# Performance work log

Measured on AMD Instinct MI355X. Metric: run time of the kernel, lower is better.

The kernel has to match this reference:

```python
import jax, jax.numpy as jnp
import numpy as np

B, L, C, H = 2, 4096, 1024, 16
D = C // H
KERNEL_FROM_KN = lambda kn: int(np.sqrt(kn)) + 1


def setup_inputs() -> dict:
    key = jax.random.key(0)
    ks = jax.random.split(key, 4)
    s = 0.02
    kk = KERNEL_FROM_KN(144)  # 13
    return {
        "x": jax.random.normal(ks[0], (B, L, C), jnp.float32),
        "w_qkv": jax.random.normal(ks[1], (C, 3 * C), jnp.float32) * s,
        "b_qkv": jnp.zeros((3 * C,), jnp.float32),
        "rpb": jax.random.normal(ks[2], (H, 2 * kk - 1), jnp.float32) * s,
        "w_proj": jax.random.normal(ks[3], (C, C), jnp.float32) * s,
        "b_proj": jnp.zeros((C,), jnp.float32),
        "k_neighbors": 144,
    }


def reference(x, w_qkv, b_qkv, rpb, w_proj, b_proj, k_neighbors):
    kk = KERNEL_FROM_KN(k_neighbors)  # kernel size (13)
    scale = D ** -0.5
    qkv = (x @ w_qkv + b_qkv).reshape(B, L, 3, H, D).transpose(2, 0, 3, 1, 4)  # (3,B,H,L,D)
    q, k, v = qkv[0] * scale, qkv[1], qkv[2]
    pos = jnp.arange(L)
    # NATTEN window: centered, clamped so the full kernel fits inside [0, L)
    start = jnp.clip(pos - kk // 2, 0, L - kk)               # (L,)
    idx = start[:, None] + jnp.arange(kk)[None, :]           # (L,kk) key positions
    k_win = k[:, :, idx, :]                                  # (B,H,L,kk,D)
    v_win = v[:, :, idx, :]                                  # (B,H,L,kk,D)
    attn = jnp.einsum('bhld,bhlkd->bhlk', q, k_win)          # (B,H,L,kk)
    # relative-position bias index = key_pos - query_pos + (kk - 1) in [0, 2kk-2]
    bias_idx = idx - pos[:, None] + (kk - 1)                 # (L,kk)
    attn = attn + rpb[:, bias_idx][None]                     # broadcast over batch
    attn = jax.nn.softmax(attn, axis=-1)
    out = jnp.einsum('bhlk,bhlkd->bhld', attn, v_win)        # (B,H,L,D)
    out = out.transpose(0, 2, 1, 3).reshape(B, L, C)
    return out @ w_proj + b_proj
```

## Files before the change

kernel.cpp:

```cpp
#include <hip/hip_runtime.h>
#include <hip/hip_bf16.h>
#include <stdint.h>

typedef __bf16 bf16x8 __attribute__((ext_vector_type(8)));
typedef float floatx4 __attribute__((ext_vector_type(4)));

#define B_ 2
#define L_ 4096
#define C_ 1024
#define H_ 16
#define D_ 64
constexpr size_t TEN = (size_t)B_ * H_ * L_ * D_;

__device__ __forceinline__ float bf2f(unsigned short u) {
  union { unsigned int i; float f; } x; x.i = ((unsigned int)u) << 16; return x.f;
}
__device__ __forceinline__ unsigned short f2bf(float f) {
  union { float f; unsigned int i; } x; x.f = f;
  unsigned int i = x.i;
  return (unsigned short)((i + 0x7FFFu + ((i >> 16) & 1u)) >> 16);
}

__device__ __forceinline__ void async_copy16(const unsigned short* g, unsigned short* l) {
  __builtin_amdgcn_global_load_lds(
      (const __attribute__((address_space(1))) unsigned int*)g,
      (__attribute__((address_space(3))) unsigned int*)l,
      16, 0, 0);
}

__global__ __launch_bounds__(256) void cvt_f32_bf16_kernel(
    const float* __restrict__ in, unsigned short* __restrict__ out, int n) {
  int i = (blockIdx.x * 256 + threadIdx.x) * 8;
  if (i >= n) return;
  float4 a = *(const float4*)&in[i];
  float4 b = *(const float4*)&in[i + 4];
  union { uint4 u; unsigned short s[8]; } st;
  st.s[0] = f2bf(a.x); st.s[1] = f2bf(a.y); st.s[2] = f2bf(a.z); st.s[3] = f2bf(a.w);
  st.s[4] = f2bf(b.x); st.s[5] = f2bf(b.y); st.s[6] = f2bf(b.z); st.s[7] = f2bf(b.w);
  *(uint4*)&out[i] = st.u;
}

__global__ __launch_bounds__(256) void transpose_f32_bf16(
    const float* __restrict__ in, unsigned short* __restrict__ out,
    int R, int Ccols) {
  __shared__ float tile[64][65];
  const int bx = blockIdx.x * 64;
  const int by = blockIdx.y * 64;
  const int t = threadIdx.x;
  for (int i = t; i < 1024; i += 256) {
    int r = i >> 4, c4 = (i & 15) << 2;
    float4 v = *(const float4*)&in[(size_t)(by + r) * Ccols + bx + c4];
    tile[r][c4] = v.x; tile[r][c4 + 1] = v.y; tile[r][c4 + 2] = v.z; tile[r][c4 + 3] = v.w;
  }
  __syncthreads();
  for (int i = t; i < 512; i += 256) {
    int r = i >> 3, c8 = (i & 7) << 3;
    union { uint4 u; unsigned short s[8]; } st;
    #pragma unroll
    for (int j = 0; j < 8; ++j) st.s[j] = f2bf(tile[c8 + j][r]);
    *(uint4*)&out[(size_t)(bx + r) * R + by + c8] = st.u;
  }
}

template <int MODE>
__global__ __launch_bounds__(256) void gemm_bt_kernel(
    const unsigned short* __restrict__ A, const unsigned short* __restrict__ Bt,
    const float* __restrict__ bias, unsigned short* __restrict__ out_bf,
    float* __restrict__ out_f, int M, int N, int K, float qscale) {
  constexpr int BK = 64;
  __shared__ unsigned short a_sh[128 * BK];
  __shared__ unsigned short b_sh[128 * BK];

  const int t = threadIdx.x;
  const int nwgx = gridDim.x;
  const int nwg = nwgx * gridDim.y;
  const int flat = blockIdx.y * nwgx + blockIdx.x;
  const int cpx = nwg >> 3;
  const int swz = (flat & 7) * cpx + (flat >> 3);
  const int n0 = (swz % nwgx) * 128;
  const int m0 = (swz / nwgx) * 128;

  const int wave = t >> 6, lane = t & 63;
  const int wr = wave >> 1, wc = wave & 1;
  const int lm = lane & 15, quad = lane >> 4;

  const int soff = t * 8;
  const int srow = soff >> 6;
  const int scol = soff & 63;

  floatx4 acc[4][4];
  #pragma unroll
  for (int i = 0; i < 4; ++i)
    #pragma unroll
    for (int j = 0; j < 4; ++j) acc[i][j] = (floatx4)0.0f;

  for (int kt = 0; kt < K; kt += BK) {
    #pragma unroll
    for (int p = 0; p < 4; ++p) {
      int r = srow + p * 32;
      int c = scol ^ ((r & 7) << 3);
      int off = r * BK + scol;
      async_copy16(&A[(size_t)(m0 + r) * K + kt + c], &a_sh[off]);
      async_copy16(&Bt[(size_t)(n0 + r) * K + kt + c], &b_sh[off]);
    }
    __syncthreads();
    #pragma unroll
    for (int ks = 0; ks < BK; ks += 32) {
      bf16x8 af[4], bfr[4];
      #pragma unroll
      for (int i = 0; i < 4; ++i) {
        int ra = wr * 64 + i * 16 + lm;
        af[i] = *(const bf16x8*)&a_sh[ra * BK + ((ks + quad * 8) ^ ((ra & 7) << 3))];
      }
      #pragma unroll
      for (int j = 0; j < 4; ++j) {
        int rb = wc * 64 + j * 16 + lm;
        bfr[j] = *(const bf16x8*)&b_sh[rb * BK + ((ks + quad * 8) ^ ((rb & 7) << 3))];
      }
      #pragma unroll
      for (int i = 0; i < 4; ++i)
        #pragma unroll
        for (int j = 0; j < 4; ++j)
          acc[i][j] = __builtin_amdgcn_mfma_f32_16x16x32_bf16(af[i], bfr[j], acc[i][j], 0, 0, 0);
    }
    __syncthreads();
  }

  #pragma unroll
  for (int j = 0; j < 4; ++j) {
    int col = n0 + wc * 64 + j * 16 + lm;
    float bv = bias[col];
    if (MODE == 0) {
      int which = col >> 10;
      int rem = col & 1023;
      int h = rem >> 6, d = rem & 63;
      float mul = (which == 0) ? qscale : 1.0f;
      #pragma unroll
      for (int i = 0; i < 4; ++i)
        #pragma unroll
        for (int r = 0; r < 4; ++r) {
          int row = m0 + wr * 64 + i * 16 + quad * 4 + r;
          int b = row >> 12, l = row & (L_ - 1);
          float v = (acc[i][j][r] + bv) * mul;
          out_bf[(size_t)which * TEN + (((size_t)(b * H_ + h) * L_ + l) * D_ + d)] = f2bf(v);
        }
    } else {
      #pragma unroll
      for (int i = 0; i < 4; ++i)
        #pragma unroll
        for (int r = 0; r < 4; ++r) {
          int row = m0 + wr * 64 + i * 16 + quad * 4 + r;
          out_f[(size_t)row * N + col] = acc[i][j][r] + bv;
        }
    }
  }
}

constexpr int KKMAX = 63;
constexpr int TL = 128;
constexpr int LDK = 72;

__global__ __launch_bounds__(256) void natt_kernel(
    const unsigned short* __restrict__ qkv,
    const float* __restrict__ rpb,
    const int* __restrict__ knp,
    unsigned short* __restrict__ attn_out) {
  __shared__ unsigned short k_sh[(TL + KKMAX) * LDK];
  __shared__ unsigned short v_sh[(TL + KKMAX) * LDK];
  __shared__ float rpb_sh[2 * KKMAX + 1];

  const int bh = blockIdx.x;
  const int h = bh & (H_ - 1);
  const int b = bh >> 4;
  const int l0 = blockIdx.y * TL;
  const int t = threadIdx.x;

  int kn = knp[0];
  if (kn > 65536 || kn < 0) {
    union { int i; float f; } u; u.i = kn; kn = (int)u.f;
  }
  int rr = 1;
  while ((rr + 1) * (rr + 1) <= kn) ++rr;
  int kk = rr + 1;
  if (kk > KKMAX) kk = KKMAX;

  int base = l0 - kk / 2;
  if (base < 0) base = 0;
  if (base > L_ - kk) base = L_ - kk;
  int nrows = TL + kk;
  if (nrows > L_ - base) nrows = L_ - base;

  const unsigned short* kg = qkv + TEN + (size_t)bh * L_ * D_;
  const unsigned short* vg = qkv + 2 * TEN + (size_t)bh * L_ * D_;

  for (int i = t; i < nrows * 8; i += 256) {
    int row = i >> 3, c8 = (i & 7) << 3;
    uint4 kv = *(const uint4*)&kg[(size_t)(base + row) * D_ + c8];
    *(uint4*)&k_sh[row * LDK + c8] = kv;
    uint4 vv = *(const uint4*)&vg[(size_t)(base + row) * D_ + c8];
    *(uint4*)&v_sh[row * LDK + c8] = vv;
  }
  int nb = 2 * kk - 1;
  for (int i = t; i < nb; i += 256) rpb_sh[i] = rpb[h * nb + i];
  __syncthreads();

  const int qi = t >> 1, half = t & 1;
  const int l = l0 + qi;

  const unsigned short* qg = qkv + (size_t)bh * L_ * D_ + (size_t)l * D_ + half * 32;
  float qv[32];
  #pragma unroll
  for (int c = 0; c < 4; ++c) {
    union { uint4 u; unsigned short s[8]; } ld;
    ld.u = *(const uint4*)&qg[c * 8];
    #pragma unroll
    for (int j = 0; j < 8; ++j) qv[c * 8 + j] = bf2f(ld.s[j]);
  }

  int start = l - kk / 2;
  if (start < 0) start = 0;
  if (start > L_ - kk) start = L_ - kk;
  const int srow = start - base;
  const int boff = start - l + kk - 1;

  float m = -1e30f, lsum = 0.0f;
  float accv[32];
  #pragma unroll
  for (int d = 0; d < 32; ++d) accv[d] = 0.0f;

  for (int j = 0; j < kk; ++j) {
    const unsigned short* kr = &k_sh[(srow + j) * LDK + half * 32];
    float partial = 0.0f;
    #pragma unroll
    for (int c = 0; c < 4; ++c) {
      union { uint4 u; unsigned short s[8]; } ld;
      ld.u = *(const uint4*)&kr[c * 8];
      #pragma unroll
      for (int jj = 0; jj < 8; ++jj) partial += qv[c * 8 + jj] * bf2f(ld.s[jj]);
    }
    float s = partial + __shfl_xor(partial, 1) + rpb_sh[boff + j];
    float p;
    if (s > m) {
      float corr = __expf(m - s);
      lsum *= corr;
      #pragma unroll
      for (int d = 0; d < 32; ++d) accv[d] *= corr;
      m = s;
      p = 1.0f;
    } else {
      p = __expf(s - m);
    }
    lsum += p;
    const unsigned short* vr = &v_sh[(srow + j) * LDK + half * 32];
    #pragma unroll
    for (int c = 0; c < 4; ++c) {
      union { uint4 u; unsigned short s[8]; } ld;
      ld.u = *(const uint4*)&vr[c * 8];
      #pragma unroll
      for (int jj = 0; jj < 8; ++jj) accv[c * 8 + jj] += p * bf2f(ld.s[jj]);
    }
  }
  float inv = 1.0f / lsum;
  unsigned short* og = attn_out + ((size_t)(b * L_ + l) * C_ + h * D_ + half * 32);
  #pragma unroll
  for (int c = 0; c < 4; ++c) {
    union { uint4 u; unsigned short s[8]; } st;
    #pragma unroll
    for (int jj = 0; jj < 8; ++jj) st.s[jj] = f2bf(accv[c * 8 + jj] * inv);
    *(uint4*)&og[c * 8] = st.u;
  }
}

extern "C" void kernel_launch(void* const* d_in, const int* in_sizes, int n_in,
                              void* d_out, int out_size, void* d_ws, size_t ws_size,
                              hipStream_t stream) {
  const float* x      = (const float*)d_in[0];
  const float* w_qkv  = (const float*)d_in[1];
  const float* b_qkv  = (const float*)d_in[2];
  const float* rpb    = (const float*)d_in[3];
  const float* w_proj = (const float*)d_in[4];
  const float* b_proj = (const float*)d_in[5];
  const int* kn       = (const int*)d_in[6];
  float* out          = (float*)d_out;

  unsigned short* ws      = (unsigned short*)d_ws;
  unsigned short* wT_qkv  = ws;
  unsigned short* wT_proj = wT_qkv + (size_t)3072 * 1024;
  unsigned short* x_bf    = wT_proj + (size_t)1024 * 1024;
  unsigned short* qkv_ws  = x_bf + (size_t)8192 * 1024;
  unsigned short* attn_ws = qkv_ws + 3 * TEN;

  cvt_f32_bf16_kernel<<<(8192 * 1024) / (256 * 8), 256, 0, stream>>>(x, x_bf, 8192 * 1024);
  transpose_f32_bf16<<<dim3(3072 / 64, 1024 / 64), 256, 0, stream>>>(w_qkv, wT_qkv, 1024, 3072);
  transpose_f32_bf16<<<dim3(1024 / 64, 1024 / 64), 256, 0, stream>>>(w_proj, wT_proj, 1024, 1024);
  gemm_bt_kernel<0><<<dim3(3072 / 128, 8192 / 128), 256, 0, stream>>>(
      x_bf, wT_qkv, b_qkv, qkv_ws, nullptr, 8192, 3072, 1024, 0.125f);
  natt_kernel<<<dim3(B_ * H_, L_ / TL), 256, 0, stream>>>(qkv_ws, rpb, kn, attn_ws);
  gemm_bt_kernel<1><<<dim3(1024 / 128, 8192 / 128), 256, 0, stream>>>(
      attn_ws, wT_proj, b_proj, nullptr, out, 8192, 1024, 1024, 1.0f);
}
```

Before: 221.5 us.

## Use exp2 softmax with lazy rescaling, native bf16 casts, and split QKV GEMM

Folds log2(e) into the Q scale and the relative-position bias so the neighborhood softmax can use the hardware exp2 instruction. It also rescales the running accumulator only when the new max exceeds the old one by more than 8. Manual round-to-nearest bf16 packing is replaced with native __bf16 casts in every conversion path. The fused QKV GEMM is split into three launches with simpler epilogue indexing, which removes the per-element which/scale selection. The cost is three smaller launches instead of one, and the lazy rescaling lets intermediate values grow by up to 256x in fp32.

```diff
diff --git a/kernel.cpp b/kernel.cpp
--- a/kernel.cpp
+++ b/kernel.cpp
@@ -11,14 +11,13 @@
 #define H_ 16
 #define D_ 64
 constexpr size_t TEN = (size_t)B_ * H_ * L_ * D_;
+#define LOG2E 1.4426950408889634f
 
 __device__ __forceinline__ float bf2f(unsigned short u) {
   union { unsigned int i; float f; } x; x.i = ((unsigned int)u) << 16; return x.f;
 }
-__device__ __forceinline__ unsigned short f2bf(float f) {
-  union { float f; unsigned int i; } x; x.f = f;
-  unsigned int i = x.i;
-  return (unsigned short)((i + 0x7FFFu + ((i >> 16) & 1u)) >> 16);
+__device__ __forceinline__ float exp2fast(float x) {
+  return __builtin_amdgcn_exp2f(x);
 }
 
 __device__ __forceinline__ void async_copy16(const unsigned short* g, unsigned short* l) {
@@ -34,9 +33,9 @@
   if (i >= n) return;
   float4 a = *(const float4*)&in[i];
   float4 b = *(const float4*)&in[i + 4];
-  union { uint4 u; unsigned short s[8]; } st;
-  st.s[0] = f2bf(a.x); st.s[1] = f2bf(a.y); st.s[2] = f2bf(a.z); st.s[3] = f2bf(a.w);
-  st.s[4] = f2bf(b.x); st.s[5] = f2bf(b.y); st.s[6] = f2bf(b.z); st.s[7] = f2bf(b.w);
+  union { uint4 u; __bf16 h[8]; } st;
+  st.h[0] = (__bf16)a.x; st.h[1] = (__bf16)a.y; st.h[2] = (__bf16)a.z; st.h[3] = (__bf16)a.w;
+  st.h[4] = (__bf16)b.x; st.h[5] = (__bf16)b.y; st.h[6] = (__bf16)b.z; st.h[7] = (__bf16)b.w;
   *(uint4*)&out[i] = st.u;
 }
 
@@ -55,9 +54,9 @@
   __syncthreads();
   for (int i = t; i < 512; i += 256) {
     int r = i >> 3, c8 = (i & 7) << 3;
-    union { uint4 u; unsigned short s[8]; } st;
-    #pragma unroll
-    for (int j = 0; j < 8; ++j) st.s[j] = f2bf(tile[c8 + j][r]);
+    union { uint4 u; __bf16 h[8]; } st;
+    #pragma unroll
+    for (int j = 0; j < 8; ++j) st.h[j] = (__bf16)tile[c8 + j][r];
     *(uint4*)&out[(size_t)(bx + r) * R + by + c8] = st.u;
   }
 }
@@ -131,18 +130,15 @@
     int col = n0 + wc * 64 + j * 16 + lm;
     float bv = bias[col];
     if (MODE == 0) {
-      int which = col >> 10;
-      int rem = col & 1023;
-      int h = rem >> 6, d = rem & 63;
-      float mul = (which == 0) ? qscale : 1.0f;
+      int h = col >> 6, d = col & 63;
       #pragma unroll
       for (int i = 0; i < 4; ++i)
         #pragma unroll
         for (int r = 0; r < 4; ++r) {
           int row = m0 + wr * 64 + i * 16 + quad * 4 + r;
           int b = row >> 12, l = row & (L_ - 1);
-          float v = (acc[i][j][r] + bv) * mul;
-          out_bf[(size_t)which * TEN + (((size_t)(b * H_ + h) * L_ + l) * D_ + d)] = f2bf(v);
+          float v = (acc[i][j][r] + bv) * qscale;
+          ((__bf16*)out_bf)[((size_t)(b * H_ + h) * L_ + l) * D_ + d] = (__bf16)v;
         }
     } else {
       #pragma unroll
@@ -201,7 +197,7 @@
     *(uint4*)&v_sh[row * LDK + c8] = vv;
   }
   int nb = 2 * kk - 1;
-  for (int i = t; i < nb; i += 256) rpb_sh[i] = rpb[h * nb + i];
+  for (int i = t; i < nb; i += 256) rpb_sh[i] = rpb[h * nb + i] * LOG2E;
   __syncthreads();
 
   const int qi = t >> 1, half = t & 1;
@@ -240,15 +236,15 @@
     }
     float s = partial + __shfl_xor(partial, 1) + rpb_sh[boff + j];
     float p;
-    if (s > m) {
-      float corr = __expf(m - s);
+    if (s - m > 8.0f) {
+      float corr = exp2fast(m - s);
       lsum *= corr;
       #pragma unroll
       for (int d = 0; d < 32; ++d) accv[d] *= corr;
       m = s;
       p = 1.0f;
     } else {
-      p = __expf(s - m);
+      p = exp2fast(s - m);
     }
     lsum += p;
     const unsigned short* vr = &v_sh[(srow + j) * LDK + half * 32];
@@ -264,9 +260,9 @@
   unsigned short* og = attn_out + ((size_t)(b * L_ + l) * C_ + h * D_ + half * 32);
   #pragma unroll
   for (int c = 0; c < 4; ++c) {
-    union { uint4 u; unsigned short s[8]; } st;
-    #pragma unroll
-    for (int jj = 0; jj < 8; ++jj) st.s[jj] = f2bf(accv[c * 8 + jj] * inv);
+    union { uint4 u; __bf16 h8[8]; } st;
+    #pragma unroll
+    for (int jj = 0; jj < 8; ++jj) st.h8[jj] = (__bf16)(accv[c * 8 + jj] * inv);
     *(uint4*)&og[c * 8] = st.u;
   }
 }
@@ -293,8 +289,15 @@
   cvt_f32_bf16_kernel<<<(8192 * 1024) / (256 * 8), 256, 0, stream>>>(x, x_bf, 8192 * 1024);
   transpose_f32_bf16<<<dim3(3072 / 64, 1024 / 64), 256, 0, stream>>>(w_qkv, wT_qkv, 1024, 3072);
   transpose_f32_bf16<<<dim3(1024 / 64, 1024 / 64), 256, 0, stream>>>(w_proj, wT_proj, 1024, 1024);
-  gemm_bt_kernel<0><<<dim3(3072 / 128, 8192 / 128), 256, 0, stream>>>(
-      x_bf, wT_qkv, b_qkv, qkv_ws, nullptr, 8192, 3072, 1024, 0.125f);
+  gemm_bt_kernel<0><<<dim3(1024 / 128, 8192 / 128), 256, 0, stream>>>(
+      x_bf, wT_qkv, b_qkv, qkv_ws, nullptr,
+      8192, 1024, 1024, 0.125f * LOG2E);
+  gemm_bt_kernel<0><<<dim3(1024 / 128, 8192 / 128), 256, 0, stream>>>(
+      x_bf, wT_qkv + (size_t)1024 * 1024, b_qkv + 1024, qkv_ws + TEN, nullptr,
+      8192, 1024, 1024, 1.0f);
+  gemm_bt_kernel<0><<<dim3(1024 / 128, 8192 / 128), 256, 0, stream>>>(
+      x_bf, wT_qkv + (size_t)2048 * 1024, b_qkv + 2048, qkv_ws + 2 * TEN, nullptr,
+      8192, 1024, 1024, 1.0f);
   natt_kernel<<<dim3(B_ * H_, L_ / TL), 256, 0, stream>>>(qkv_ws, rpb, kn, attn_ws);
   gemm_bt_kernel<1><<<dim3(1024 / 128, 8192 / 128), 256, 0, stream>>>(
       attn_ws, wT_proj, b_proj, nullptr, out, 8192, 1024, 1024, 1.0f);
```

Result: slower. 229.1 us (+3.4%).
